# Kernel tuning notes

Measured on AMD Instinct MI355X. Metric: run time of the kernel, lower is better.

## Reference

```python
import jax, jax.numpy as jnp
import numpy as np

N = 50000
E = 800000
IN_DIM = 512
H1 = IN_DIM // 2   # 256
H2 = IN_DIM // 4   # 128
D = 8
NP_CAYLEY = D * (D - 1) // 2  # 28


def setup_inputs() -> dict:
    key = jax.random.key(0)
    ks = jax.random.split(key, 10)
    x = jax.random.normal(ks[0], (N, IN_DIM), dtype=jnp.float32)
    edge_index = jax.random.randint(ks[1], (2, E), 0, N, dtype=jnp.int64)
    s1 = 1.0 / np.sqrt(IN_DIM)
    s2 = 1.0 / np.sqrt(H1)
    s3 = 1.0 / np.sqrt(H2)
    W1l = jax.random.uniform(ks[2], (H1, IN_DIM), jnp.float32, -s1, s1)
    b1 = jax.random.uniform(ks[3], (H1,), jnp.float32, -s1, s1)
    W1r = jax.random.uniform(ks[4], (H1, IN_DIM), jnp.float32, -s1, s1)
    W2l = jax.random.uniform(ks[5], (H2, H1), jnp.float32, -s2, s2)
    b2 = jax.random.uniform(ks[6], (H2,), jnp.float32, -s2, s2)
    W2r = jax.random.uniform(ks[7], (H2, H1), jnp.float32, -s2, s2)
    Wp = jax.random.uniform(ks[8], (NP_CAYLEY, H2), jnp.float32, -s3, s3)
    bp = jax.random.uniform(ks[9], (NP_CAYLEY,), jnp.float32, -s3, s3)
    return {"x": x, "edge_index": edge_index,
            "W1l": W1l, "b1": b1, "W1r": W1r,
            "W2l": W2l, "b2": b2, "W2r": W2r,
            "Wp": Wp, "bp": bp}


def _sage_conv(x, src, dst, Wl, bl, Wr):
    # PyG SAGEConv (mean aggr): out = lin_l(mean_{j in N(i)} x_j) + lin_r(x_i)
    msg_sum = jax.ops.segment_sum(x[src], dst, num_segments=N)  # [N, F]
    deg = jax.ops.segment_sum(jnp.ones((src.shape[0],), x.dtype), dst,
                              num_segments=N)
    mean = msg_sum / jnp.maximum(deg, 1.0)[:, None]
    return mean @ Wl.T + bl + x @ Wr.T


def _cayley(params):
    # params: [N, d(d-1)/2] -> skew A, then O = (I - A)^{-1} (I + A)
    iu, ju = jnp.triu_indices(D, k=1)  # row-major i<j matches torch loop order
    n = params.shape[0]
    A = jnp.zeros((n, D, D), params.dtype)
    A = A.at[:, iu, ju].set(params)
    A = A.at[:, ju, iu].set(-params)
    I = jnp.eye(D, dtype=params.dtype)
    return jnp.linalg.solve(I[None] - A, I[None] + A)


def reference(x, edge_index, W1l, b1, W1r, W2l, b2, W2r, Wp, bp):
    src, dst = edge_index[0], edge_index[1]
    h = jax.nn.relu(_sage_conv(x, src, dst, W1l, b1, W1r))
    h = jax.nn.relu(_sage_conv(h, src, dst, W2l, b2, W2r))
    params = h @ Wp.T + bp  # [N, 28]
    return _cayley(params)  # [N, 8, 8]
```

## Files before the change

kernel.cpp:

```cpp
#include <hip/hip_runtime.h>
#include <hip/hip_bf16.h>


#define WS_ALIGN(x) (((x) + 255) & ~size_t(255))

typedef __attribute__((ext_vector_type(8))) short short8;
typedef __attribute__((ext_vector_type(4))) float floatx4;

static __device__ __forceinline__ ushort f2b(float f) {
    unsigned u = __builtin_bit_cast(unsigned, f);
    u = (u + 0x7fffu + ((u >> 16) & 1u)) >> 16;
    return (ushort)u;
}
static __device__ __forceinline__ float b2f(ushort h) {
    unsigned u = ((unsigned)h) << 16;
    return __builtin_bit_cast(float, u);
}
static __device__ __forceinline__ unsigned pk2(float a, float b) {
    return (unsigned)f2b(a) | ((unsigned)f2b(b) << 16);
}


__global__ void hist_kernel(const int* __restrict__ dst, int* __restrict__ deg, int E) {
    int e = blockIdx.x * blockDim.x + threadIdx.x;
    if (e < E) atomicAdd(&deg[dst[e]], 1);
}

__global__ __launch_bounds__(256)
void scan_phase1(const int* __restrict__ deg, int* __restrict__ bsum, int n) {
    __shared__ int red[256];
    const int t = threadIdx.x;
    const int i = blockIdx.x * 1024 + t * 4;
    int s = 0;
    if (i + 4 <= n) {
        int4 v = *reinterpret_cast<const int4*>(&deg[i]);
        s = v.x + v.y + v.z + v.w;
    } else {
        for (int k = i; k < n; ++k) s += deg[k];
    }
    red[t] = s;
    __syncthreads();
#pragma unroll
    for (int off = 128; off > 0; off >>= 1) {
        if (t < off) red[t] += red[t + off];
        __syncthreads();
    }
    if (t == 0) bsum[blockIdx.x] = red[0];
}

__global__ __launch_bounds__(256)
void scan_phase2(int* __restrict__ bsum, int* __restrict__ rowptr, int nb, int n) {
    __shared__ int sh[256];
    const int t = threadIdx.x;
    int orig = (t < nb) ? bsum[t] : 0;
    sh[t] = orig;
    __syncthreads();
#pragma unroll
    for (int off = 1; off < 256; off <<= 1) {
        int v = (t >= off) ? sh[t - off] : 0;
        __syncthreads();
        sh[t] += v;
        __syncthreads();
    }
    if (t < nb) bsum[t] = sh[t] - orig;
    if (t == 255) rowptr[n] = sh[255];
}

__global__ __launch_bounds__(256)
void scan_phase3(const int* __restrict__ deg, const int* __restrict__ bsum,
                 int* __restrict__ rowptr, int n) {
    __shared__ int red[256];
    const int t = threadIdx.x;
    const int i = blockIdx.x * 1024 + t * 4;
    int v0 = 0, v1 = 0, v2 = 0, v3 = 0;
    if (i + 4 <= n) {
        int4 v = *reinterpret_cast<const int4*>(&deg[i]);
        v0 = v.x; v1 = v.y; v2 = v.z; v3 = v.w;
    } else {
        if (i     < n) v0 = deg[i];
        if (i + 1 < n) v1 = deg[i + 1];
        if (i + 2 < n) v2 = deg[i + 2];
        if (i + 3 < n) v3 = deg[i + 3];
    }
    int s = v0 + v1 + v2 + v3;
    red[t] = s;
    __syncthreads();
#pragma unroll
    for (int off = 1; off < 256; off <<= 1) {
        int u = (t >= off) ? red[t - off] : 0;
        __syncthreads();
        red[t] += u;
        __syncthreads();
    }
    int pre = bsum[blockIdx.x] + red[t] - s;
    if (i + 4 <= n) {
        int4 o;
        o.x = pre; o.y = pre + v0; o.z = pre + v0 + v1; o.w = pre + v0 + v1 + v2;
        *reinterpret_cast<int4*>(&rowptr[i]) = o;
    } else {
        if (i     < n) rowptr[i]     = pre;
        if (i + 1 < n) rowptr[i + 1] = pre + v0;
        if (i + 2 < n) rowptr[i + 2] = pre + v0 + v1;
        if (i + 3 < n) rowptr[i + 3] = pre + v0 + v1 + v2;
    }
}

__global__ void scatter_kernel(const int* __restrict__ src, const int* __restrict__ dst,
                               const int* __restrict__ rowptr, int* __restrict__ cursor,
                               int* __restrict__ adj, int E) {
    int e = blockIdx.x * blockDim.x + threadIdx.x;
    if (e < E) {
        int d = dst[e];
        int p = atomicAdd(&cursor[d], 1);
        adj[rowptr[d] + p] = src[e];
    }
}

__global__ void build_wcat(const float* __restrict__ W1l, const float* __restrict__ W1r,
                           const float* __restrict__ W2l, const float* __restrict__ W2r,
                           ushort* __restrict__ Wc1, ushort* __restrict__ Wc2) {
    int idx = blockIdx.x * blockDim.x + threadIdx.x;
    const int n1 = (512 * 512) / 8;
    const int n2 = (256 * 256) / 8;
    const float* src;
    ushort* dst;
    if (idx < n1) {
        int e = idx * 8;
        int row = e >> 9, col = e & 511;
        src = (row < 256) ? &W1l[row * 512 + col] : &W1r[(row - 256) * 512 + col];
        dst = &Wc1[e];
    } else if (idx < n1 + n2) {
        int e = (idx - n1) * 8;
        int row = e >> 8, col = e & 255;
        src = (row < 128) ? &W2l[row * 256 + col] : &W2r[(row - 128) * 256 + col];
        dst = &Wc2[e];
    } else {
        return;
    }
    const float4* s4 = reinterpret_cast<const float4*>(src);
    float4 v0 = s4[0], v1 = s4[1];
    short8 o;
    o[0] = (short)f2b(v0.x); o[1] = (short)f2b(v0.y);
    o[2] = (short)f2b(v0.z); o[3] = (short)f2b(v0.w);
    o[4] = (short)f2b(v1.x); o[5] = (short)f2b(v1.y);
    o[6] = (short)f2b(v1.z); o[7] = (short)f2b(v1.w);
    *reinterpret_cast<short8*>(dst) = o;
}


template <bool CASTA>
__global__ __launch_bounds__(512, 4)
void gemm_wide(const float* __restrict__ Af, const ushort* __restrict__ Ab,
               const ushort* __restrict__ B,
               ushort* __restrict__ Cl, ushort* __restrict__ Cr,
               int M, int K, int Ncols, int S) {
    __shared__ ushort As[128 * 64];
    __shared__ ushort Bs[256 * 64];
    const int tid  = threadIdx.x;
    const int wave = tid >> 6;
    const int lane = tid & 63;
    const int row0 = blockIdx.y * 128;
    const int col0 = blockIdx.x * 256;
    const int wm = (wave & 1) * 64;
    const int wn = (wave >> 1) * 64;

    floatx4 acc[4][4];
#pragma unroll
    for (int i = 0; i < 4; ++i)
#pragma unroll
        for (int j = 0; j < 4; ++j)
            acc[i][j] = (floatx4){0.f, 0.f, 0.f, 0.f};

    const int rsub = lane >> 3;
    const int ksw  = ((lane & 7) * 16) ^ (rsub << 4);

    const int ar = tid >> 2;
    const int aq = tid & 3;
    int agrow = row0 + ar; if (agrow >= M) agrow = M - 1;
    const float* arow_base = CASTA ? (Af + (size_t)agrow * K + aq * 16) : nullptr;
    char* alds = (char*)As + ar * 128;
    const int arx = (ar & 7) << 4;

    float4 va0, va1, va2, va3;
    if constexpr (CASTA) {
        const float* s0 = arow_base;
        va0 = *reinterpret_cast<const float4*>(s0 + 0);
        va1 = *reinterpret_cast<const float4*>(s0 + 4);
        va2 = *reinterpret_cast<const float4*>(s0 + 8);
        va3 = *reinterpret_cast<const float4*>(s0 + 12);
    }

    for (int k0 = 0; k0 < K; k0 += 64) {
#pragma unroll
        for (int i = 0; i < 4; ++i) {
            int chunk = wave * 4 + i;
            int r = chunk * 8 + rsub;
            int gcol = col0 + r;
            const char* src = (const char*)(B + (size_t)gcol * K + k0) + ksw;
            __builtin_amdgcn_global_load_lds(
                (const __attribute__((address_space(1))) unsigned int*)src,
                (__attribute__((address_space(3))) unsigned int*)(&Bs[chunk * 512]),
                16, 0, 0);
        }
        if constexpr (CASTA) {
            uint4 o0 = make_uint4(pk2(va0.x, va0.y), pk2(va0.z, va0.w),
                                  pk2(va1.x, va1.y), pk2(va1.z, va1.w));
            uint4 o1 = make_uint4(pk2(va2.x, va2.y), pk2(va2.z, va2.w),
                                  pk2(va3.x, va3.y), pk2(va3.z, va3.w));
            int g0 = aq * 2;
            *reinterpret_cast<uint4*>(alds + ((g0 * 16) ^ arx))       = o0;
            *reinterpret_cast<uint4*>(alds + (((g0 + 1) * 16) ^ arx)) = o1;
            if (k0 + 64 < K) {
                const float* s1 = arow_base + k0 + 64;
                va0 = *reinterpret_cast<const float4*>(s1 + 0);
                va1 = *reinterpret_cast<const float4*>(s1 + 4);
                va2 = *reinterpret_cast<const float4*>(s1 + 8);
                va3 = *reinterpret_cast<const float4*>(s1 + 12);
            }
        } else {
#pragma unroll
            for (int i = 0; i < 2; ++i) {
                int chunk = wave * 2 + i;
                int r = chunk * 8 + rsub;
                int grow = row0 + r;
                if (grow >= M) grow = M - 1;
                const char* src = (const char*)(Ab + (size_t)grow * K + k0) + ksw;
                __builtin_amdgcn_global_load_lds(
                    (const __attribute__((address_space(1))) unsigned int*)src,
                    (__attribute__((address_space(3))) unsigned int*)(&As[chunk * 512]),
                    16, 0, 0);
            }
        }
        __syncthreads();

#pragma unroll
        for (int kk = 0; kk < 2; ++kk) {
            short8 af[4], bf[4];
            const int kb = (kk * 64 + ((lane >> 4) << 4)) ^ ((lane & 7) << 4);
#pragma unroll
            for (int im = 0; im < 4; ++im) {
                int r = wm + im * 16 + (lane & 15);
                af[im] = *reinterpret_cast<const short8*>((const char*)As + r * 128 + kb);
            }
#pragma unroll
            for (int in = 0; in < 4; ++in) {
                int r = wn + in * 16 + (lane & 15);
                bf[in] = *reinterpret_cast<const short8*>((const char*)Bs + r * 128 + kb);
            }
#pragma unroll
            for (int im = 0; im < 4; ++im)
#pragma unroll
                for (int in = 0; in < 4; ++in)
                    acc[im][in] = __builtin_amdgcn_mfma_f32_16x16x32_bf16(
                        af[im], bf[in], acc[im][in], 0, 0, 0);
        }
        __syncthreads();
    }

#pragma unroll
    for (int im = 0; im < 4; ++im) {
#pragma unroll
        for (int reg = 0; reg < 4; ++reg) {
            int r = row0 + wm + im * 16 + ((lane >> 4) << 2) + reg;
            if (r < M) {
#pragma unroll
                for (int in = 0; in < 4; ++in) {
                    int g = col0 + wn + in * 16 + (lane & 15);
                    if (g < S) Cl[(size_t)r * S + g] = f2b(acc[im][in][reg]);
                    else       Cr[(size_t)r * S + (g - S)] = f2b(acc[im][in][reg]);
                }
            }
        }
    }
}


template <int LPN>
__global__ __launch_bounds__(256)
void aggregate_bf16(const ushort* __restrict__ Yl, const ushort* __restrict__ Yr,
                    const float* __restrict__ bias,
                    const int* __restrict__ rowptr, const int* __restrict__ adj,
                    ushort* __restrict__ H, int n) {
    constexpr int F = LPN * 8;
    const int grp = threadIdx.x / LPN;
    const int sub = threadIdx.x % LPN;
    const int node = blockIdx.x * (256 / LPN) + grp;
    if (node >= n) return;
    const int c = sub * 8;
    const int start = rowptr[node], end = rowptr[node + 1];

    float acc[8];
#pragma unroll
    for (int v = 0; v < 8; ++v) acc[v] = 0.f;

    int e = start;
    for (; e + 4 <= end; e += 4) {
        int s0 = adj[e + 0], s1 = adj[e + 1], s2 = adj[e + 2], s3 = adj[e + 3];
        short8 r0 = *reinterpret_cast<const short8*>(&Yl[(size_t)s0 * F + c]);
        short8 r1 = *reinterpret_cast<const short8*>(&Yl[(size_t)s1 * F + c]);
        short8 r2 = *reinterpret_cast<const short8*>(&Yl[(size_t)s2 * F + c]);
        short8 r3 = *reinterpret_cast<const short8*>(&Yl[(size_t)s3 * F + c]);
#pragma unroll
        for (int v = 0; v < 8; ++v)
            acc[v] += (b2f((ushort)r0[v]) + b2f((ushort)r1[v])) +
                      (b2f((ushort)r2[v]) + b2f((ushort)r3[v]));
    }
    for (; e < end; ++e) {
        int s = adj[e];
        short8 r = *reinterpret_cast<const short8*>(&Yl[(size_t)s * F + c]);
#pragma unroll
        for (int v = 0; v < 8; ++v) acc[v] += b2f((ushort)r[v]);
    }

    const int d = end - start;
    const float inv = 1.0f / (float)(d > 0 ? d : 1);
    short8 sv = *reinterpret_cast<const short8*>(&Yr[(size_t)node * F + c]);
    float4 bv0 = *reinterpret_cast<const float4*>(&bias[c]);
    float4 bv1 = *reinterpret_cast<const float4*>(&bias[c + 4]);
    float bb[8] = {bv0.x, bv0.y, bv0.z, bv0.w, bv1.x, bv1.y, bv1.z, bv1.w};
    short8 o;
#pragma unroll
    for (int v = 0; v < 8; ++v)
        o[v] = (short)f2b(fmaxf(acc[v] * inv + b2f((ushort)sv[v]) + bb[v], 0.f));
    *reinterpret_cast<short8*>(&H[(size_t)node * F + c]) = o;
}


__global__ __launch_bounds__(256)
void params_kernel(const ushort* __restrict__ H2, const float* __restrict__ Wp,
                   const float* __restrict__ bp, float* __restrict__ P, int n) {
    __shared__ float WpS[32 * 132];
    __shared__ float bpS[32];
    for (int t = threadIdx.x; t < 32 * 132; t += 256) WpS[t] = 0.f;
    if (threadIdx.x < 32) bpS[threadIdx.x] = (threadIdx.x < 28) ? bp[threadIdx.x] : 0.f;
    __syncthreads();
    for (int t = threadIdx.x; t < 28 * 128; t += 256) {
        int r = t >> 7, c = t & 127;
        WpS[r * 132 + c] = Wp[t];
    }
    __syncthreads();

    const int node = blockIdx.x * 32 + (threadIdx.x >> 3);
    const int l = threadIdx.x & 7;
    if (node >= n) return;

    short8 h8[16];
    const short8* hp = reinterpret_cast<const short8*>(&H2[(size_t)node * 128]);
#pragma unroll
    for (int q = 0; q < 16; ++q) h8[q] = hp[q];

    float acc0 = bpS[l], acc1 = bpS[l + 8], acc2 = bpS[l + 16], acc3 = bpS[l + 24];
#pragma unroll
    for (int q = 0; q < 32; ++q) {
        float h0 = b2f((ushort)h8[q >> 1][(q & 1) * 4 + 0]);
        float h1 = b2f((ushort)h8[q >> 1][(q & 1) * 4 + 1]);
        float h2 = b2f((ushort)h8[q >> 1][(q & 1) * 4 + 2]);
        float h3 = b2f((ushort)h8[q >> 1][(q & 1) * 4 + 3]);
        float4 w0 = *reinterpret_cast<const float4*>(&WpS[(l +  0) * 132 + 4 * q]);
        float4 w1 = *reinterpret_cast<const float4*>(&WpS[(l +  8) * 132 + 4 * q]);
        float4 w2 = *reinterpret_cast<const float4*>(&WpS[(l + 16) * 132 + 4 * q]);
        float4 w3 = *reinterpret_cast<const float4*>(&WpS[(l + 24) * 132 + 4 * q]);
        acc0 += h0 * w0.x + h1 * w0.y + h2 * w0.z + h3 * w0.w;
        acc1 += h0 * w1.x + h1 * w1.y + h2 * w1.z + h3 * w1.w;
        acc2 += h0 * w2.x + h1 * w2.y + h2 * w2.z + h3 * w2.w;
        acc3 += h0 * w3.x + h1 * w3.y + h2 * w3.z + h3 * w3.w;
    }
    float* pout = &P[(size_t)node * 32];
    pout[l]      = acc0;
    pout[l + 8]  = acc1;
    pout[l + 16] = acc2;
    pout[l + 24] = acc3;
}


__global__ __launch_bounds__(256)
void cayley_kernel(const float* __restrict__ P, float* __restrict__ Out, int n) {
    int i = blockIdx.x * blockDim.x + threadIdx.x;
    if (i >= n) return;
    float p[28];
    const float4* pp = reinterpret_cast<const float4*>(&P[(size_t)i * 32]);
#pragma unroll
    for (int q = 0; q < 7; ++q) {
        float4 v = pp[q];
        p[4 * q + 0] = v.x; p[4 * q + 1] = v.y;
        p[4 * q + 2] = v.z; p[4 * q + 3] = v.w;
    }

    float M_[8][8], B_[8][8];
#pragma unroll
    for (int r = 0; r < 8; ++r)
#pragma unroll
        for (int c = 0; c < 8; ++c) {
            M_[r][c] = (r == c) ? 1.f : 0.f;
            B_[r][c] = (r == c) ? 1.f : 0.f;
        }
    {
        int idx = 0;
#pragma unroll
        for (int r = 0; r < 8; ++r)
#pragma unroll
            for (int c = r + 1; c < 8; ++c) {
                float a = p[idx++];
                M_[r][c] -= a;  M_[c][r] += a;
                B_[r][c] += a;  B_[c][r] -= a;
            }
    }
#pragma unroll
    for (int col = 0; col < 8; ++col) {
        float inv = 1.0f / M_[col][col];
#pragma unroll
        for (int c = 0; c < 8; ++c) { M_[col][c] *= inv; B_[col][c] *= inv; }
#pragma unroll
        for (int r = 0; r < 8; ++r) {
            if (r == col) continue;
            float f = M_[r][col];
#pragma unroll
            for (int c = 0; c < 8; ++c) {
                M_[r][c] -= f * M_[col][c];
                B_[r][c] -= f * B_[col][c];
            }
        }
    }
    float* out = &Out[(size_t)i * 64];
#pragma unroll
    for (int r = 0; r < 8; ++r) {
        float4 o0 = make_float4(B_[r][0], B_[r][1], B_[r][2], B_[r][3]);
        float4 o1 = make_float4(B_[r][4], B_[r][5], B_[r][6], B_[r][7]);
        *reinterpret_cast<float4*>(&out[r * 8 + 0]) = o0;
        *reinterpret_cast<float4*>(&out[r * 8 + 4]) = o1;
    }
}


extern "C" void kernel_launch(void* const* d_in, const int* in_sizes, int n_in,
                              void* d_out, int out_size, void* d_ws, size_t ws_size,
                              hipStream_t stream) {
    const float* x   = (const float*)d_in[0];
    const int*   ei  = (const int*)d_in[1];
    const float* W1l = (const float*)d_in[2];
    const float* b1  = (const float*)d_in[3];
    const float* W1r = (const float*)d_in[4];
    const float* W2l = (const float*)d_in[5];
    const float* b2  = (const float*)d_in[6];
    const float* W2r = (const float*)d_in[7];
    const float* Wp  = (const float*)d_in[8];
    const float* bp  = (const float*)d_in[9];
    float* out = (float*)d_out;

    const int IN_DIM = 512;
    const int N = in_sizes[0] / IN_DIM;
    const int E = in_sizes[1] / 2;

    char* ws = (char*)d_ws;
    size_t off = 0;
    int* deg      = (int*)(ws + off); off = WS_ALIGN(off + (size_t)N * 4);
    int* rowptr   = (int*)(ws + off); off = WS_ALIGN(off + (size_t)(N + 1) * 4);
    int* cursor   = (int*)(ws + off); off = WS_ALIGN(off + (size_t)N * 4);
    int* bsum     = (int*)(ws + off); off = WS_ALIGN(off + (size_t)256 * 4);
    int* adj      = (int*)(ws + off); off = WS_ALIGN(off + (size_t)E * 4);
    ushort* Yl    = (ushort*)(ws + off); off = WS_ALIGN(off + (size_t)N * 256 * 2);
    ushort* Yr    = (ushort*)(ws + off); off = WS_ALIGN(off + (size_t)N * 256 * 2);
    ushort* h1    = (ushort*)(ws + off); off = WS_ALIGN(off + (size_t)N * 256 * 2);
    ushort* zl    = (ushort*)(ws + off); off = WS_ALIGN(off + (size_t)N * 128 * 2);
    ushort* zr    = (ushort*)(ws + off); off = WS_ALIGN(off + (size_t)N * 128 * 2);
    ushort* Wc1   = (ushort*)(ws + off); off = WS_ALIGN(off + (size_t)512 * 512 * 2);
    ushort* Wc2   = (ushort*)(ws + off); off = WS_ALIGN(off + (size_t)256 * 256 * 2);
    float*  Pp    = (float*)(ws + off);  off = WS_ALIGN(off + (size_t)N * 32 * 4);

    const int* src = ei;
    const int* dst = ei + E;

    hipMemsetAsync(deg, 0, (size_t)N * 4, stream);
    hipMemsetAsync(cursor, 0, (size_t)N * 4, stream);

    int eb = (E + 255) / 256;
    int nb = (N + 1023) / 1024;
    hist_kernel<<<eb, 256, 0, stream>>>(dst, deg, E);
    scan_phase1<<<nb, 256, 0, stream>>>(deg, bsum, N);
    scan_phase2<<<1, 256, 0, stream>>>(bsum, rowptr, nb, N);
    scan_phase3<<<nb, 256, 0, stream>>>(deg, bsum, rowptr, N);
    scatter_kernel<<<eb, 256, 0, stream>>>(src, dst, rowptr, cursor, adj, E);

    build_wcat<<<((512 * 512 + 256 * 256) / 8 + 255) / 256, 256, 0, stream>>>(
        W1l, W1r, W2l, W2r, Wc1, Wc2);

    int gm = (N + 127) / 128;

    gemm_wide<true><<<dim3(2, gm), 512, 0, stream>>>(
        x, (const ushort*)nullptr, Wc1, Yl, Yr, N, 512, 512, 256);
    aggregate_bf16<32><<<(N + 7) / 8, 256, 0, stream>>>(Yl, Yr, b1, rowptr, adj, h1, N);

    gemm_wide<false><<<dim3(1, gm), 512, 0, stream>>>(
        (const float*)nullptr, h1, Wc2, zl, zr, N, 256, 256, 128);
    ushort* h2 = Yl;
    aggregate_bf16<16><<<(N + 15) / 16, 256, 0, stream>>>(zl, zr, b2, rowptr, adj, h2, N);

    params_kernel<<<(N + 31) / 32, 256, 0, stream>>>(h2, Wp, bp, Pp, N);
    cayley_kernel<<<(N + 255) / 256, 256, 0, stream>>>(Pp, out, N);
}
```

Baseline: 276.7 us.

## Double-buffer GEMM LDS tiles with smaller 128x128 blocks

Replaces the single-buffered 128x256 GEMM tile (512 threads) with a double-buffered 128x128 tile (256 threads). The next K-slice is prefetched into the alternate LDS buffer while MFMAs run on the current one, which removes one barrier per iteration and hides global load latency. The grid grows to 4 and 2 column blocks, so the fp32 A rows of the first layer are read and converted to bf16 four times instead of twice, in exchange for more blocks and better latency hiding. The output store also drops the per-element left/right branch because each block now lies entirely on one side.

```diff
diff --git a/kernel.cpp b/kernel.cpp
--- a/kernel.cpp
+++ b/kernel.cpp
@@ -149,18 +149,18 @@
 
 
 template <bool CASTA>
-__global__ __launch_bounds__(512, 4)
-void gemm_wide(const float* __restrict__ Af, const ushort* __restrict__ Ab,
-               const ushort* __restrict__ B,
-               ushort* __restrict__ Cl, ushort* __restrict__ Cr,
-               int M, int K, int Ncols, int S) {
-    __shared__ ushort As[128 * 64];
-    __shared__ ushort Bs[256 * 64];
+__global__ __launch_bounds__(256)
+void gemm_db(const float* __restrict__ Af, const ushort* __restrict__ Ab,
+             const ushort* __restrict__ B,
+             ushort* __restrict__ Cl, ushort* __restrict__ Cr,
+             int M, int K, int Ncols, int S) {
+    __shared__ ushort As[2][128 * 64];
+    __shared__ ushort Bs[2][128 * 64];
     const int tid  = threadIdx.x;
     const int wave = tid >> 6;
     const int lane = tid & 63;
     const int row0 = blockIdx.y * 128;
-    const int col0 = blockIdx.x * 256;
+    const int col0 = blockIdx.x * 128;
     const int wm = (wave & 1) * 64;
     const int wn = (wave >> 1) * 64;
 
@@ -174,65 +174,97 @@
     const int rsub = lane >> 3;
     const int ksw  = ((lane & 7) * 16) ^ (rsub << 4);
 
-    const int ar = tid >> 2;
-    const int aq = tid & 3;
+    const int ar = tid >> 1, ah = tid & 1;
     int agrow = row0 + ar; if (agrow >= M) agrow = M - 1;
-    const float* arow_base = CASTA ? (Af + (size_t)agrow * K + aq * 16) : nullptr;
-    char* alds = (char*)As + ar * 128;
+    const float* arow = CASTA ? (Af + (size_t)agrow * K + ah * 32) : nullptr;
     const int arx = (ar & 7) << 4;
-
-    float4 va0, va1, va2, va3;
+    float4 va[8];
+
     if constexpr (CASTA) {
-        const float* s0 = arow_base;
-        va0 = *reinterpret_cast<const float4*>(s0 + 0);
-        va1 = *reinterpret_cast<const float4*>(s0 + 4);
-        va2 = *reinterpret_cast<const float4*>(s0 + 8);
-        va3 = *reinterpret_cast<const float4*>(s0 + 12);
-    }
-
-    for (int k0 = 0; k0 < K; k0 += 64) {
+#pragma unroll
+        for (int j = 0; j < 8; ++j)
+            va[j] = *reinterpret_cast<const float4*>(arow + j * 4);
+    }
+#pragma unroll
+    for (int i = 0; i < 4; ++i) {
+        int chunk = wave * 4 + i;
+        int r = chunk * 8 + rsub;
+        int gcol = col0 + r;
+        const char* srcp = (const char*)(B + (size_t)gcol * K) + ksw;
+        __builtin_amdgcn_global_load_lds(
+            (const __attribute__((address_space(1))) unsigned int*)srcp,
+            (__attribute__((address_space(3))) unsigned int*)(&Bs[0][chunk * 512]),
+            16, 0, 0);
+    }
+    if constexpr (CASTA) {
+        char* alds = (char*)&As[0][0] + ar * 128;
+#pragma unroll
+        for (int g = 0; g < 4; ++g) {
+            uint4 o = make_uint4(pk2(va[2 * g].x, va[2 * g].y),
+                                 pk2(va[2 * g].z, va[2 * g].w),
+                                 pk2(va[2 * g + 1].x, va[2 * g + 1].y),
+                                 pk2(va[2 * g + 1].z, va[2 * g + 1].w));
+            *reinterpret_cast<uint4*>(alds + (((ah * 4 + g) * 16) ^ arx)) = o;
+        }
+    } else {
 #pragma unroll
         for (int i = 0; i < 4; ++i) {
             int chunk = wave * 4 + i;
             int r = chunk * 8 + rsub;
-            int gcol = col0 + r;
-            const char* src = (const char*)(B + (size_t)gcol * K + k0) + ksw;
+            int grow = row0 + r;
+            if (grow >= M) grow = M - 1;
+            const char* srcp = (const char*)(Ab + (size_t)grow * K) + ksw;
             __builtin_amdgcn_global_load_lds(
-                (const __attribute__((address_space(1))) unsigned int*)src,
-                (__attribute__((address_space(3))) unsigned int*)(&Bs[chunk * 512]),
+                (const __attribute__((address_space(1))) unsigned int*)srcp,
+                (__attribute__((address_space(3))) unsigned int*)(&As[0][chunk * 512]),
                 16, 0, 0);
         }
-        if constexpr (CASTA) {
-            uint4 o0 = make_uint4(pk2(va0.x, va0.y), pk2(va0.z, va0.w),
-                                  pk2(va1.x, va1.y), pk2(va1.z, va1.w));
-            uint4 o1 = make_uint4(pk2(va2.x, va2.y), pk2(va2.z, va2.w),
-                                  pk2(va3.x, va3.y), pk2(va3.z, va3.w));
-            int g0 = aq * 2;
-            *reinterpret_cast<uint4*>(alds + ((g0 * 16) ^ arx))       = o0;
-            *reinterpret_cast<uint4*>(alds + (((g0 + 1) * 16) ^ arx)) = o1;
-            if (k0 + 64 < K) {
-                const float* s1 = arow_base + k0 + 64;
-                va0 = *reinterpret_cast<const float4*>(s1 + 0);
-                va1 = *reinterpret_cast<const float4*>(s1 + 4);
-                va2 = *reinterpret_cast<const float4*>(s1 + 8);
-                va3 = *reinterpret_cast<const float4*>(s1 + 12);
-            }
-        } else {
-#pragma unroll
-            for (int i = 0; i < 2; ++i) {
-                int chunk = wave * 2 + i;
+    }
+    __syncthreads();
+
+    const int nt = K >> 6;
+    int cur = 0;
+#pragma unroll 2
+    for (int t = 0; t < nt; ++t) {
+        const int k0 = t * 64;
+        const int nxt = cur ^ 1;
+        const bool more = (t + 1 < nt);
+
+        if (more) {
+#pragma unroll
+            for (int i = 0; i < 4; ++i) {
+                int chunk = wave * 4 + i;
                 int r = chunk * 8 + rsub;
-                int grow = row0 + r;
-                if (grow >= M) grow = M - 1;
-                const char* src = (const char*)(Ab + (size_t)grow * K + k0) + ksw;
+                int gcol = col0 + r;
+                const char* srcp = (const char*)(B + (size_t)gcol * K + k0 + 64) + ksw;
                 __builtin_amdgcn_global_load_lds(
-                    (const __attribute__((address_space(1))) unsigned int*)src,
-                    (__attribute__((address_space(3))) unsigned int*)(&As[chunk * 512]),
+                    (const __attribute__((address_space(1))) unsigned int*)srcp,
+                    (__attribute__((address_space(3))) unsigned int*)(&Bs[nxt][chunk * 512]),
                     16, 0, 0);
             }
-        }
-        __syncthreads();
-
+            if constexpr (CASTA) {
+                const float* s1 = arow + k0 + 64;
+#pragma unroll
+                for (int j = 0; j < 8; ++j)
+                    va[j] = *reinterpret_cast<const float4*>(s1 + j * 4);
+            } else {
+#pragma unroll
+                for (int i = 0; i < 4; ++i) {
+                    int chunk = wave * 4 + i;
+                    int r = chunk * 8 + rsub;
+                    int grow = row0 + r;
+                    if (grow >= M) grow = M - 1;
+                    const char* srcp = (const char*)(Ab + (size_t)grow * K + k0 + 64) + ksw;
+                    __builtin_amdgcn_global_load_lds(
+                        (const __attribute__((address_space(1))) unsigned int*)srcp,
+                        (__attribute__((address_space(3))) unsigned int*)(&As[nxt][chunk * 512]),
+                        16, 0, 0);
+                }
+            }
+        }
+
+        const char* Al = (const char*)&As[cur][0];
+        const char* Bl = (const char*)&Bs[cur][0];
 #pragma unroll
         for (int kk = 0; kk < 2; ++kk) {
             short8 af[4], bf[4];
@@ -240,12 +272,12 @@
 #pragma unroll
             for (int im = 0; im < 4; ++im) {
                 int r = wm + im * 16 + (lane & 15);
-                af[im] = *reinterpret_cast<const short8*>((const char*)As + r * 128 + kb);
+                af[im] = *reinterpret_cast<const short8*>(Al + r * 128 + kb);
             }
 #pragma unroll
             for (int in = 0; in < 4; ++in) {
                 int r = wn + in * 16 + (lane & 15);
-                bf[in] = *reinterpret_cast<const short8*>((const char*)Bs + r * 128 + kb);
+                bf[in] = *reinterpret_cast<const short8*>(Bl + r * 128 + kb);
             }
 #pragma unroll
             for (int im = 0; im < 4; ++im)
@@ -254,21 +286,34 @@
                     acc[im][in] = __builtin_amdgcn_mfma_f32_16x16x32_bf16(
                         af[im], bf[in], acc[im][in], 0, 0, 0);
         }
+
+        if (CASTA && more) {
+            char* alds = (char*)&As[cur ^ 1][0] + ar * 128;
+#pragma unroll
+            for (int g = 0; g < 4; ++g) {
+                uint4 o = make_uint4(pk2(va[2 * g].x, va[2 * g].y),
+                                     pk2(va[2 * g].z, va[2 * g].w),
+                                     pk2(va[2 * g + 1].x, va[2 * g + 1].y),
+                                     pk2(va[2 * g + 1].z, va[2 * g + 1].w));
+                *reinterpret_cast<uint4*>(alds + (((ah * 4 + g) * 16) ^ arx)) = o;
+            }
+        }
         __syncthreads();
-    }
-
+        cur ^= 1;
+    }
+
+    ushort* Cbase = (col0 < S) ? Cl : Cr;
+    const int cb = (col0 < S) ? col0 : col0 - S;
 #pragma unroll
     for (int im = 0; im < 4; ++im) {
 #pragma unroll
         for (int reg = 0; reg < 4; ++reg) {
             int r = row0 + wm + im * 16 + ((lane >> 4) << 2) + reg;
             if (r < M) {
-#pragma unroll
-                for (int in = 0; in < 4; ++in) {
-                    int g = col0 + wn + in * 16 + (lane & 15);
-                    if (g < S) Cl[(size_t)r * S + g] = f2b(acc[im][in][reg]);
-                    else       Cr[(size_t)r * S + (g - S)] = f2b(acc[im][in][reg]);
-                }
+                size_t base = (size_t)r * S + cb + wn + (lane & 15);
+#pragma unroll
+                for (int in = 0; in < 4; ++in)
+                    Cbase[base + in * 16] = f2b(acc[im][in][reg]);
             }
         }
     }
@@ -486,11 +531,11 @@
 
     int gm = (N + 127) / 128;
 
-    gemm_wide<true><<<dim3(2, gm), 512, 0, stream>>>(
+    gemm_db<true><<<dim3(4, gm), 256, 0, stream>>>(
         x, (const ushort*)nullptr, Wc1, Yl, Yr, N, 512, 512, 256);
     aggregate_bf16<32><<<(N + 7) / 8, 256, 0, stream>>>(Yl, Yr, b1, rowptr, adj, h1, N);
 
-    gemm_wide<false><<<dim3(1, gm), 512, 0, stream>>>(
+    gemm_db<false><<<dim3(2, gm), 256, 0, stream>>>(
         (const float*)nullptr, h1, Wc2, zl, zr, N, 256, 256, 128);
     ushort* h2 = Yl;
     aggregate_bf16<16><<<(N + 15) / 16, 256, 0, stream>>>(zl, zr, b2, rowptr, adj, h2, N);
```

After: 317.4 us. 1.15x slower.

## Fuse layer-2 aggregation with params projection and merge prep kernels

Applied to the files above, without the earlier changes.

The second mean aggregation is fused with the 128->28 projection, so h2 is never written to or read back from global memory. Each 16-lane group computes partial dot products and reduces them with xor shuffles. The degree histogram and the bf16 weight conversion are merged into one launch, and the cursor memset is folded into scan_phase3. Together these remove launches and an intermediate round trip, at the cost of heavier shuffle work per node in the fused kernel.

```diff
diff --git a/kernel.cpp b/kernel.cpp
--- a/kernel.cpp
+++ b/kernel.cpp
@@ -21,10 +21,46 @@
 }
 
 
-__global__ void hist_kernel(const int* __restrict__ dst, int* __restrict__ deg, int E) {
-    int e = blockIdx.x * blockDim.x + threadIdx.x;
-    if (e < E) atomicAdd(&deg[dst[e]], 1);
-}
+__global__ __launch_bounds__(256)
+void prep_kernel(const int* __restrict__ dst, int* __restrict__ deg, int E, int eb,
+                 const float* __restrict__ W1l, const float* __restrict__ W1r,
+                 const float* __restrict__ W2l, const float* __restrict__ W2r,
+                 ushort* __restrict__ Wc1, ushort* __restrict__ Wc2) {
+    const int b = blockIdx.x;
+    const int tid = threadIdx.x;
+    if (b < eb) {
+        int e = b * 256 + tid;
+        if (e < E) atomicAdd(&deg[dst[e]], 1);
+    } else {
+        int idx = (b - eb) * 256 + tid;
+        const int n1 = (512 * 512) / 8;
+        const int n2 = (256 * 256) / 8;
+        const float* src;
+        ushort* dstp;
+        if (idx < n1) {
+            int e = idx * 8;
+            int row = e >> 9, col = e & 511;
+            src = (row < 256) ? &W1l[row * 512 + col] : &W1r[(row - 256) * 512 + col];
+            dstp = &Wc1[e];
+        } else if (idx < n1 + n2) {
+            int e = (idx - n1) * 8;
+            int row = e >> 8, col = e & 255;
+            src = (row < 128) ? &W2l[row * 256 + col] : &W2r[(row - 128) * 256 + col];
+            dstp = &Wc2[e];
+        } else {
+            return;
+        }
+        const float4* s4 = reinterpret_cast<const float4*>(src);
+        float4 v0 = s4[0], v1 = s4[1];
+        short8 o;
+        o[0] = (short)f2b(v0.x); o[1] = (short)f2b(v0.y);
+        o[2] = (short)f2b(v0.z); o[3] = (short)f2b(v0.w);
+        o[4] = (short)f2b(v1.x); o[5] = (short)f2b(v1.y);
+        o[6] = (short)f2b(v1.z); o[7] = (short)f2b(v1.w);
+        *reinterpret_cast<short8*>(dstp) = o;
+    }
+}
+
 
 __global__ __launch_bounds__(256)
 void scan_phase1(const int* __restrict__ deg, int* __restrict__ bsum, int n) {
@@ -68,7 +104,7 @@
 
 __global__ __launch_bounds__(256)
 void scan_phase3(const int* __restrict__ deg, const int* __restrict__ bsum,
-                 int* __restrict__ rowptr, int n) {
+                 int* __restrict__ rowptr, int* __restrict__ cursor, int n) {
     __shared__ int red[256];
     const int t = threadIdx.x;
     const int i = blockIdx.x * 1024 + t * 4;
@@ -97,11 +133,12 @@
         int4 o;
         o.x = pre; o.y = pre + v0; o.z = pre + v0 + v1; o.w = pre + v0 + v1 + v2;
         *reinterpret_cast<int4*>(&rowptr[i]) = o;
+        *reinterpret_cast<int4*>(&cursor[i]) = make_int4(0, 0, 0, 0);
     } else {
-        if (i     < n) rowptr[i]     = pre;
-        if (i + 1 < n) rowptr[i + 1] = pre + v0;
-        if (i + 2 < n) rowptr[i + 2] = pre + v0 + v1;
-        if (i + 3 < n) rowptr[i + 3] = pre + v0 + v1 + v2;
+        if (i     < n) { rowptr[i]     = pre;              cursor[i]     = 0; }
+        if (i + 1 < n) { rowptr[i + 1] = pre + v0;         cursor[i + 1] = 0; }
+        if (i + 2 < n) { rowptr[i + 2] = pre + v0 + v1;    cursor[i + 2] = 0; }
+        if (i + 3 < n) { rowptr[i + 3] = pre + v0 + v1 + v2; cursor[i + 3] = 0; }
     }
 }
 
@@ -114,37 +151,6 @@
         int p = atomicAdd(&cursor[d], 1);
         adj[rowptr[d] + p] = src[e];
     }
-}
-
-__global__ void build_wcat(const float* __restrict__ W1l, const float* __restrict__ W1r,
-                           const float* __restrict__ W2l, const float* __restrict__ W2r,
-                           ushort* __restrict__ Wc1, ushort* __restrict__ Wc2) {
-    int idx = blockIdx.x * blockDim.x + threadIdx.x;
-    const int n1 = (512 * 512) / 8;
-    const int n2 = (256 * 256) / 8;
-    const float* src;
-    ushort* dst;
-    if (idx < n1) {
-        int e = idx * 8;
-        int row = e >> 9, col = e & 511;
-        src = (row < 256) ? &W1l[row * 512 + col] : &W1r[(row - 256) * 512 + col];
-        dst = &Wc1[e];
-    } else if (idx < n1 + n2) {
-        int e = (idx - n1) * 8;
-        int row = e >> 8, col = e & 255;
-        src = (row < 128) ? &W2l[row * 256 + col] : &W2r[(row - 128) * 256 + col];
-        dst = &Wc2[e];
-    } else {
-        return;
-    }
-    const float4* s4 = reinterpret_cast<const float4*>(src);
-    float4 v0 = s4[0], v1 = s4[1];
-    short8 o;
-    o[0] = (short)f2b(v0.x); o[1] = (short)f2b(v0.y);
-    o[2] = (short)f2b(v0.z); o[3] = (short)f2b(v0.w);
-    o[4] = (short)f2b(v1.x); o[5] = (short)f2b(v1.y);
-    o[6] = (short)f2b(v1.z); o[7] = (short)f2b(v1.w);
-    *reinterpret_cast<short8*>(dst) = o;
 }
 
 
@@ -327,49 +333,79 @@
 
 
 __global__ __launch_bounds__(256)
-void params_kernel(const ushort* __restrict__ H2, const float* __restrict__ Wp,
-                   const float* __restrict__ bp, float* __restrict__ P, int n) {
-    __shared__ float WpS[32 * 132];
-    __shared__ float bpS[32];
-    for (int t = threadIdx.x; t < 32 * 132; t += 256) WpS[t] = 0.f;
-    if (threadIdx.x < 32) bpS[threadIdx.x] = (threadIdx.x < 28) ? bp[threadIdx.x] : 0.f;
+void agg2_params(const ushort* __restrict__ Zl, const ushort* __restrict__ Zr,
+                 const float* __restrict__ bias,
+                 const int* __restrict__ rowptr, const int* __restrict__ adj,
+                 const float* __restrict__ Wp, const float* __restrict__ bp,
+                 float* __restrict__ P, int n) {
+    constexpr int F = 128;
+    __shared__ float WpS[28 * 128];
+    __shared__ float bpS[28];
+    for (int t = threadIdx.x; t < 28 * 128; t += 256) WpS[t] = Wp[t];
+    if (threadIdx.x < 28) bpS[threadIdx.x] = bp[threadIdx.x];
     __syncthreads();
-    for (int t = threadIdx.x; t < 28 * 128; t += 256) {
-        int r = t >> 7, c = t & 127;
-        WpS[r * 132 + c] = Wp[t];
-    }
-    __syncthreads();
-
-    const int node = blockIdx.x * 32 + (threadIdx.x >> 3);
-    const int l = threadIdx.x & 7;
+
+    const int grp = threadIdx.x >> 4;
+    const int sub = threadIdx.x & 15;
+    const int node = blockIdx.x * 16 + grp;
     if (node >= n) return;
-
-    short8 h8[16];
-    const short8* hp = reinterpret_cast<const short8*>(&H2[(size_t)node * 128]);
-#pragma unroll
-    for (int q = 0; q < 16; ++q) h8[q] = hp[q];
-
-    float acc0 = bpS[l], acc1 = bpS[l + 8], acc2 = bpS[l + 16], acc3 = bpS[l + 24];
-#pragma unroll
-    for (int q = 0; q < 32; ++q) {
-        float h0 = b2f((ushort)h8[q >> 1][(q & 1) * 4 + 0]);
-        float h1 = b2f((ushort)h8[q >> 1][(q & 1) * 4 + 1]);
-        float h2 = b2f((ushort)h8[q >> 1][(q & 1) * 4 + 2]);
-        float h3 = b2f((ushort)h8[q >> 1][(q & 1) * 4 + 3]);
-        float4 w0 = *reinterpret_cast<const float4*>(&WpS[(l +  0) * 132 + 4 * q]);
-        float4 w1 = *reinterpret_cast<const float4*>(&WpS[(l +  8) * 132 + 4 * q]);
-        float4 w2 = *reinterpret_cast<const float4*>(&WpS[(l + 16) * 132 + 4 * q]);
-        float4 w3 = *reinterpret_cast<const float4*>(&WpS[(l + 24) * 132 + 4 * q]);
-        acc0 += h0 * w0.x + h1 * w0.y + h2 * w0.z + h3 * w0.w;
-        acc1 += h0 * w1.x + h1 * w1.y + h2 * w1.z + h3 * w1.w;
-        acc2 += h0 * w2.x + h1 * w2.y + h2 * w2.z + h3 * w2.w;
-        acc3 += h0 * w3.x + h1 * w3.y + h2 * w3.z + h3 * w3.w;
-    }
-    float* pout = &P[(size_t)node * 32];
-    pout[l]      = acc0;
-    pout[l + 8]  = acc1;
-    pout[l + 16] = acc2;
-    pout[l + 24] = acc3;
+    const int c = sub * 8;
+    const int start = rowptr[node], end = rowptr[node + 1];
+
+    float acc[8];
+#pragma unroll
+    for (int v = 0; v < 8; ++v) acc[v] = 0.f;
+
+    int e = start;
+    for (; e + 4 <= end; e += 4) {
+        int s0 = adj[e + 0], s1 = adj[e + 1], s2 = adj[e + 2], s3 = adj[e + 3];
+        short8 r0 = *reinterpret_cast<const short8*>(&Zl[(size_t)s0 * F + c]);
+        short8 r1 = *reinterpret_cast<const short8*>(&Zl[(size_t)s1 * F + c]);
+        short8 r2 = *reinterpret_cast<const short8*>(&Zl[(size_t)s2 * F + c]);
+        short8 r3 = *reinterpret_cast<const short8*>(&Zl[(size_t)s3 * F + c]);
+#pragma unroll
+        for (int v = 0; v < 8; ++v)
+            acc[v] += (b2f((ushort)r0[v]) + b2f((ushort)r1[v])) +
+                      (b2f((ushort)r2[v]) + b2f((ushort)r3[v]));
+    }
+    for (; e < end; ++e) {
+        int s = adj[e];
+        short8 r = *reinterpret_cast<const short8*>(&Zl[(size_t)s * F + c]);
+#pragma unroll
+        for (int v = 0; v < 8; ++v) acc[v] += b2f((ushort)r[v]);
+    }
+
+    const int d = end - start;
+    const float inv = 1.0f / (float)(d > 0 ? d : 1);
+    short8 sv = *reinterpret_cast<const short8*>(&Zr[(size_t)node * F + c]);
+    float4 bv0 = *reinterpret_cast<const float4*>(&bias[c]);
+    float4 bv1 = *reinterpret_cast<const float4*>(&bias[c + 4]);
+    float bb[8] = {bv0.x, bv0.y, bv0.z, bv0.w, bv1.x, bv1.y, bv1.z, bv1.w};
+    float hv[8];
+#pragma unroll
+    for (int v = 0; v < 8; ++v)
+        hv[v] = fmaxf(acc[v] * inv + b2f((ushort)sv[v]) + bb[v], 0.f);
+
+    float p[28];
+#pragma unroll
+    for (int j = 0; j < 28; ++j) {
+        const float* w = &WpS[j * 128 + c];
+        float4 w0 = *reinterpret_cast<const float4*>(w);
+        float4 w1 = *reinterpret_cast<const float4*>(w + 4);
+        p[j] = hv[0] * w0.x + hv[1] * w0.y + hv[2] * w0.z + hv[3] * w0.w +
+               hv[4] * w1.x + hv[5] * w1.y + hv[6] * w1.z + hv[7] * w1.w;
+    }
+#pragma unroll
+    for (int m = 8; m >= 1; m >>= 1) {
+#pragma unroll
+        for (int j = 0; j < 28; ++j)
+            p[j] += __shfl_xor(p[j], m);
+    }
+    if (sub < 14) {
+        float2 o = make_float2(p[2 * sub] + bpS[2 * sub],
+                               p[2 * sub + 1] + bpS[2 * sub + 1]);
+        *reinterpret_cast<float2*>(&P[(size_t)node * 32 + 2 * sub]) = o;
+    }
 }
 
 
@@ -471,18 +507,17 @@
     const int* dst = ei + E;
 
     hipMemsetAsync(deg, 0, (size_t)N * 4, stream);
-    hipMemsetAsync(cursor, 0, (size_t)N * 4, stream);
-
-    int eb = (E + 255) / 256;
-    int nb = (N + 1023) / 1024;
-    hist_kernel<<<eb, 256, 0, stream>>>(dst, deg, E);
+
+    const int eb = (E + 255) / 256;
+    const int wb = ((512 * 512 + 256 * 256) / 8 + 255) / 256;
+    const int nb = (N + 1023) / 1024;
+
+    prep_kernel<<<eb + wb, 256, 0, stream>>>(
+        dst, deg, E, eb, W1l, W1r, W2l, W2r, Wc1, Wc2);
     scan_phase1<<<nb, 256, 0, stream>>>(deg, bsum, N);
     scan_phase2<<<1, 256, 0, stream>>>(bsum, rowptr, nb, N);
-    scan_phase3<<<nb, 256, 0, stream>>>(deg, bsum, rowptr, N);
+    scan_phase3<<<nb, 256, 0, stream>>>(deg, bsum, rowptr, cursor, N);
     scatter_kernel<<<eb, 256, 0, stream>>>(src, dst, rowptr, cursor, adj, E);
-
-    build_wcat<<<((512 * 512 + 256 * 256) / 8 + 255) / 256, 256, 0, stream>>>(
-        W1l, W1r, W2l, W2r, Wc1, Wc2);
 
     int gm = (N + 127) / 128;
 
@@ -492,9 +527,9 @@
 
     gemm_wide<false><<<dim3(1, gm), 512, 0, stream>>>(
         (const float*)nullptr, h1, Wc2, zl, zr, N, 256, 256, 128);
-    ushort* h2 = Yl;
-    aggregate_bf16<16><<<(N + 15) / 16, 256, 0, stream>>>(zl, zr, b2, rowptr, adj, h2, N);
-
-    params_kernel<<<(N + 31) / 32, 256, 0, stream>>>(h2, Wp, bp, Pp, N);
+
+    agg2_params<<<(N + 15) / 16, 256, 0, stream>>>(
+        zl, zr, b2, rowptr, adj, Wp, bp, Pp, N);
+
     cayley_kernel<<<(N + 255) / 256, 256, 0, stream>>>(Pp, out, N);
 }
```

Result: slower. 305.0 us (+10.3%).
